# Kernel optimization log

Hardware: AMD Instinct MI355X
Metric: run time of the kernel (lower is better)

The kernel has to match this reference:

```python
import jax, jax.numpy as jnp
import numpy as np

VOCAB = 100000
EMBED = 300
HIDDEN = 300
BATCH = 32768
K_NEG = 10
N_CLASSES = 2
EPS = 1e-5
DENO_W = 1.0
CONO_W = 1.0


def setup_inputs() -> dict:
    key = jax.random.key(0)
    ks = jax.random.split(key, 12)
    init_range = 1.0 / EMBED
    return {
        "center_word_ids": jax.random.randint(ks[0], (BATCH,), 0, VOCAB),
        "context_word_ids": jax.random.randint(ks[1], (BATCH,), 0, VOCAB),
        "neg_context_ids": jax.random.randint(ks[2], (BATCH, K_NEG), 0, VOCAB),
        "party_label": jax.random.randint(ks[3], (BATCH,), 0, N_CLASSES),
        "center_emb": jax.random.uniform(ks[4], (VOCAB, EMBED), jnp.float32, -init_range, init_range),
        "context_emb": jax.random.normal(ks[5], (VOCAB, EMBED), jnp.float32) * 0.02,
        "W_enc": jax.random.normal(ks[6], (HIDDEN, EMBED), jnp.float32) * (1.0 / np.sqrt(EMBED)),
        "b_enc": jnp.zeros((HIDDEN,), jnp.float32),
        "W_dec": jax.random.normal(ks[7], (EMBED, HIDDEN), jnp.float32) * (1.0 / np.sqrt(HIDDEN)),
        "b_dec": jnp.zeros((EMBED,), jnp.float32),
        "W_cls": jax.random.normal(ks[8], (N_CLASSES, HIDDEN), jnp.float32) * (1.0 / np.sqrt(HIDDEN)),
        "b_cls": jnp.zeros((N_CLASSES,), jnp.float32),
    }


def reference(center_word_ids, context_word_ids, neg_context_ids, party_label,
              center_emb, context_emb, W_enc, b_enc, W_dec, b_dec, W_cls, b_cls):
    # encoder_forward (dropout p=0 -> identity)
    emb = center_emb[center_word_ids]                      # [B, E]
    enc = emb @ W_enc.T + b_enc                            # [B, H]
    # deno_forward: skip-gram negative sampling
    center_v = enc @ W_dec.T + b_dec                       # [B, E]
    ctx_v = context_emb[context_word_ids]                  # [B, E]
    pos_score = jnp.clip(jnp.sum(center_v * ctx_v, axis=1), -10.0, 10.0)
    pos = -jax.nn.log_sigmoid(pos_score)                   # [B]
    neg_v = context_emb[neg_context_ids]                   # [B, K, E]
    neg_score = jnp.clip(jnp.einsum('bke,be->bk', neg_v, center_v), -10.0, 10.0)
    neg = -jnp.sum(jax.nn.log_sigmoid(-neg_score), axis=1)  # [B]
    deno_loss = jnp.clip(jnp.mean(pos + neg), EPS, 10.0)
    # cono_forward + cross entropy
    logits = enc @ W_cls.T + b_cls                         # [B, C]
    logp = jax.nn.log_softmax(logits, axis=-1)
    nll = -jnp.take_along_axis(logp, party_label[:, None], axis=1)[:, 0]
    cono_loss = jnp.clip(jnp.mean(nll), EPS, 10.0)
    encoder_loss = jnp.clip(DENO_W * deno_loss + CONO_W * cono_loss, EPS, None)
    return jnp.stack([encoder_loss, deno_loss, cono_loss])
```

## Files before the change

kernel.cpp:

```cpp
#include <hip/hip_runtime.h>
#include <math.h>

#define VOCAB   100000
#define EMBED   300
#define HIDDEN  300
#define BATCH   32768
#define K_NEG   10
#define EPSV    1e-5f

#define KPAD      320
#define NPAD      384
#define CV_STRIDE 304
#define CTX8_STRIDE 304
#define WC2_STRIDE 304
#define FP8_SCALE 64.0f
#define FP8_DESCALE 0.015625f
#define NBUCKET 512

typedef __attribute__((ext_vector_type(8))) short  short8;
typedef __attribute__((ext_vector_type(4))) float  f32x4;
typedef __attribute__((ext_vector_type(2))) float  floatx2;

#if defined(__has_builtin)
#if __has_builtin(__builtin_amdgcn_cvt_pk_f32_fp8) && __has_builtin(__builtin_amdgcn_cvt_pk_fp8_f32)
#define HAVE_CVT_FP8 1
#endif
#endif

__device__ inline float b2f(unsigned short u) {
    union { unsigned int i; float f; } v; v.i = ((unsigned int)u) << 16; return v.f;
}
__device__ inline unsigned short f2b(float f) {
    union { float f; unsigned int i; } v; v.f = f;
    unsigned int r = v.i + 0x7FFFu + ((v.i >> 16) & 1u);
    return (unsigned short)(r >> 16);
}
__device__ inline void up2(unsigned int u, float& lo, float& hi) {
    union { unsigned int i; float f; } a, b;
    a.i = u << 16; b.i = u & 0xFFFF0000u;
    lo = a.f; hi = b.f;
}
__device__ inline float softplus_fast(float x) {
    const float t = __builtin_amdgcn_exp2f(fabsf(x) * -1.44269504f);
    const float l = __builtin_amdgcn_logf(1.f + t) * 0.69314718f;
    return fmaxf(x, 0.f) + l;
}

__device__ inline float fp8_to_f(unsigned int u8) {
    const unsigned s = (u8 >> 7) & 1, e = (u8 >> 3) & 15, m = u8 & 7;
    float v;
    if (e) { union { unsigned i; float f; } b; b.i = ((e + 120u) << 23) | (m << 20); v = b.f; }
    else v = (float)m * 0.001953125f;
    return s ? -v : v;
}
__device__ inline unsigned char f_to_fp8(float x) {
    union { float f; unsigned i; } b; b.f = x;
    const unsigned s = (b.i >> 31) << 7;
    const float a = fabsf(x);
    if (a >= 440.f) return (unsigned char)(s | 0x7E);
    if (a < 0.015625f) {
        int m = (int)rintf(a * 512.f);
        return (unsigned char)(m >= 8 ? (s | 0x08) : (s | (unsigned)m));
    }
    unsigned r = (b.i & 0x7FFFFFFFu) + 0x7FFFFu + ((b.i >> 20) & 1u);
    unsigned e8 = (r >> 23) - 120u;
    unsigned m8 = (r >> 20) & 7u;
    if (e8 > 15u) return (unsigned char)(s | 0x7E);
    return (unsigned char)(s | (e8 << 3) | m8);
}
__device__ inline unsigned enc4fp8(float a, float b, float c, float d) {
#ifdef HAVE_CVT_FP8
    int v = 0;
    v = __builtin_amdgcn_cvt_pk_fp8_f32(a, b, v, false);
    v = __builtin_amdgcn_cvt_pk_fp8_f32(c, d, v, true);
    return (unsigned)v;
#else
    return (unsigned)f_to_fp8(a) | ((unsigned)f_to_fp8(b) << 8) |
           ((unsigned)f_to_fp8(c) << 16) | ((unsigned)f_to_fp8(d) << 24);
#endif
}
__device__ inline void dec4fp8(unsigned u, float* f) {
#ifdef HAVE_CVT_FP8
    floatx2 lo = __builtin_amdgcn_cvt_pk_f32_fp8((int)u, false);
    floatx2 hi = __builtin_amdgcn_cvt_pk_f32_fp8((int)u, true);
    f[0] = lo[0]; f[1] = lo[1]; f[2] = hi[0]; f[3] = hi[1];
#else
    f[0] = fp8_to_f(u); f[1] = fp8_to_f(u >> 8);
    f[2] = fp8_to_f(u >> 16); f[3] = fp8_to_f(u >> 24);
#endif
}

__device__ inline void load_lds16(const void* g, void* l) {
    __builtin_amdgcn_global_load_lds(
        (const __attribute__((address_space(1))) unsigned int*)g,
        (__attribute__((address_space(3))) unsigned int*)l, 16, 0, 0);
}

__device__ inline float red64(float v) {
    #pragma unroll
    for (int m = 32; m; m >>= 1) v += __shfl_xor(v, m);
    return v;
}

__device__ inline unsigned packbf2(float lo, float hi) {
    union { float f; unsigned i; } a, b; a.f = lo; b.f = hi;
    return (b.i & 0xFFFF0000u) | (a.i >> 16);
}

#define NE (BATCH * 40)
#define NC (VOCAB * 19)

__global__ __launch_bounds__(256)
void prep_kernel(const float* __restrict__ cemb, const int* __restrict__ cids,
                 const float* __restrict__ xemb,
                 unsigned short* __restrict__ emb_b, unsigned char* __restrict__ ctx8)
{
    const int gid = blockIdx.x * 256 + threadIdx.x;
    if (gid < NE) {
        const int row = gid / 40;
        const int c8  = (gid - row * 40) * 8;
        const float* src = cemb + (size_t)cids[row] * 300;
        unsigned short t[8];
        if (c8 + 7 < 300) {
            float4 a = *(const float4*)(src + c8);
            float4 b = *(const float4*)(src + c8 + 4);
            t[0]=f2b(a.x); t[1]=f2b(a.y); t[2]=f2b(a.z); t[3]=f2b(a.w);
            t[4]=f2b(b.x); t[5]=f2b(b.y); t[6]=f2b(b.z); t[7]=f2b(b.w);
        } else {
            #pragma unroll
            for (int j = 0; j < 8; ++j) {
                const int c = c8 + j;
                t[j] = (c < 300) ? f2b(src[c]) : (unsigned short)0;
            }
        }
        *(uint4*)(emb_b + (size_t)row * KPAD + c8) = *(const uint4*)t;
    } else if (gid < NE + NC) {
        const int g3  = gid - NE;
        const int row = g3 / 19;
        const int l   = g3 - row * 19;
        const int e0  = l * 16;
        const float* src = xemb + (size_t)row * 300 + e0;
        float v[16];
        #pragma unroll
        for (int q = 0; q < 4; ++q) {
            if (e0 + q * 4 + 3 < 300) {
                float4 a = *(const float4*)(src + q * 4);
                v[q*4+0]=a.x; v[q*4+1]=a.y; v[q*4+2]=a.z; v[q*4+3]=a.w;
            } else {
                #pragma unroll
                for (int j = 0; j < 4; ++j) {
                    const int e = e0 + q * 4 + j;
                    v[q*4+j] = (e < 300) ? src[q*4+j] : 0.f;
                }
            }
        }
        unsigned u[4];
        #pragma unroll
        for (int q = 0; q < 4; ++q)
            u[q] = enc4fp8(v[q*4]*FP8_SCALE, v[q*4+1]*FP8_SCALE,
                           v[q*4+2]*FP8_SCALE, v[q*4+3]*FP8_SCALE);
        *(uint4*)(ctx8 + (size_t)row * CTX8_STRIDE + e0) = make_uint4(u[0],u[1],u[2],u[3]);
    }
}

__global__ __launch_bounds__(256)
void w2_kernel(const float* __restrict__ Wd, const float* __restrict__ We,
               unsigned short* __restrict__ w2p)
{
    __shared__ float ds[16][33];
    __shared__ float es[32][17];
    const int tid = threadIdx.x;
    const int tn = tid >> 4, tk = tid & 15;
    const int n = blockIdx.y * 16 + tn;
    const int k = blockIdx.x * 16 + tk;

    float acc = 0.f;
    for (int h0 = 0; h0 < 300; h0 += 32) {
        {
            const int i = tid * 2;
            const int a = i >> 5, h = i & 31;
            const int rr = blockIdx.y * 16 + a;
            #pragma unroll
            for (int j = 0; j < 2; ++j) {
                const int hh = h + j;
                ds[a][hh] = (rr < 300 && h0 + hh < 300) ? Wd[rr * 300 + h0 + hh] : 0.f;
            }
        }
        {
            const int i = tid * 2;
            const int h = i >> 4, c = i & 15;
            const int cc = blockIdx.x * 16 + c;
            #pragma unroll
            for (int j = 0; j < 2; ++j)
                es[h][c + j] = (h0 + h < 300 && cc + j < 300) ? We[(h0 + h) * 300 + cc + j] : 0.f;
        }
        __syncthreads();
        #pragma unroll
        for (int h = 0; h < 32; ++h)
            acc = fmaf(ds[tn][h], es[h][tk], acc);
        __syncthreads();
    }
    if (n < NPAD && k < KPAD)
        w2p[n * KPAD + k] = (n < 300 && k < 300) ? f2b(acc) : (unsigned short)0;
}

__global__ __launch_bounds__(256)
void wb_kernel(const float* __restrict__ Wd, const float* __restrict__ We,
               const float* __restrict__ Wc, const float* __restrict__ b_enc,
               const float* __restrict__ b_dec, const float* __restrict__ b_cls,
               float* __restrict__ wc2, float* __restrict__ bias2, float* __restrict__ bc2)
{
    const int unit = blockIdx.x * 4 + (threadIdx.x >> 6);
    const int lane = threadIdx.x & 63;
    if (unit >= 914) return;
    float s = 0.f;
    if (unit < 304) {
        const int c = unit;
        if (c < 300)
            for (int k = lane; k < 300; k += 64) s = fmaf(Wd[c * 300 + k], b_enc[k], s);
        s = red64(s);
        if (lane == 0) bias2[c] = (c < 300) ? s + b_dec[c] : 0.f;
    } else if (unit < 912) {
        const int u2 = unit - 304;
        const int j = u2 >= 304 ? 1 : 0;
        const int c = u2 - j * 304;
        if (c < 300)
            for (int h = lane; h < 300; h += 64) s = fmaf(Wc[j * 300 + h], We[h * 300 + c], s);
        s = red64(s);
        if (lane == 0) wc2[j * WC2_STRIDE + c] = s;
    } else {
        const int j = unit - 912;
        for (int h = lane; h < 300; h += 64) s = fmaf(Wc[j * 300 + h], b_enc[h], s);
        s = red64(s);
        if (lane == 0) bc2[j] = s + b_cls[j];
    }
}

__global__ __launch_bounds__(256)
void gemm_cv_kernel(const unsigned short* __restrict__ A,
                    const unsigned short* __restrict__ B,
                    const float* __restrict__ bias,
                    unsigned short* __restrict__ C)
{
    __shared__ unsigned short As[2][128 * 32];
    __shared__ unsigned short Bs[2][128 * 32];

    const int tid  = threadIdx.x;
    const int wave = tid >> 6;
    const int lane = tid & 63;
    const int m0 = blockIdx.y * 128;
    const int n0 = blockIdx.x * 128;

    const int wr = (wave & 1) * 64;
    const int wc = (wave >> 1) * 64;
    const int fr = lane & 15;
    const int fq = lane >> 4;

    const unsigned short* gA[2];
    const unsigned short* gB[2];
    int ldsOff[2];
    #pragma unroll
    for (int inst = 0; inst < 2; ++inst) {
        const int t = wave * 2 + inst;
        const int r = (t << 4) + (lane >> 2);
        const int c = ((lane & 3) - r - (r >> 2)) & 3;
        gA[inst] = A + (size_t)(m0 + r) * KPAD + c * 8;
        gB[inst] = B + (size_t)(n0 + r) * KPAD + c * 8;
        ldsOff[inst] = t << 9;
    }

    int aoff[4], boff[4];
    #pragma unroll
    for (int i = 0; i < 4; ++i) {
        const int ra = wr + i * 16 + fr;
        aoff[i] = (ra << 5) + (((fq + ra + (ra >> 2)) & 3) << 3);
        const int rb = wc + i * 16 + fr;
        boff[i] = (rb << 5) + (((fq + rb + (rb >> 2)) & 3) << 3);
    }

    f32x4 acc[4][4] = {};

    #pragma unroll
    for (int inst = 0; inst < 2; ++inst) {
        load_lds16(gA[inst], &As[0][ldsOff[inst]]);
        load_lds16(gB[inst], &Bs[0][ldsOff[inst]]);
    }

    int cur = 0;
    for (int ki = 0; ki < KPAD / 32; ++ki) {
        __syncthreads();
        if (ki + 1 < KPAD / 32) {
            const int k0 = (ki + 1) * 32;
            #pragma unroll
            for (int inst = 0; inst < 2; ++inst) {
                load_lds16(gA[inst] + k0, &As[cur ^ 1][ldsOff[inst]]);
                load_lds16(gB[inst] + k0, &Bs[cur ^ 1][ldsOff[inst]]);
            }
        }
        short8 af[4], bf[4];
        #pragma unroll
        for (int i = 0; i < 4; ++i) af[i] = *(const short8*)&As[cur][aoff[i]];
        #pragma unroll
        for (int j = 0; j < 4; ++j) bf[j] = *(const short8*)&Bs[cur][boff[j]];
        #pragma unroll
        for (int i = 0; i < 4; ++i)
            #pragma unroll
            for (int j = 0; j < 4; ++j)
                acc[i][j] = __builtin_amdgcn_mfma_f32_16x16x32_bf16(
                    af[i], bf[j], acc[i][j], 0, 0, 0);
        cur ^= 1;
    }

    #pragma unroll
    for (int i = 0; i < 4; ++i) {
        #pragma unroll
        for (int r = 0; r < 4; ++r) {
            const int m = m0 + wr + i * 16 + fq * 4 + r;
            unsigned short* crow = C + (size_t)m * CV_STRIDE;
            #pragma unroll
            for (int j = 0; j < 4; ++j) {
                const int n = n0 + wc + j * 16 + fr;
                if (n < 300) {
                    crow[n] = f2b(acc[i][j][r] + bias[n]);
                } else if (n < CV_STRIDE) {
                    crow[n] = 0;
                }
            }
        }
    }
}

__global__ __launch_bounds__(256)
void score_kernel(const unsigned short* __restrict__ cvb,
                  const unsigned char* __restrict__ ctx8,
                  const int* __restrict__ ctx_ids, const int* __restrict__ neg_ids,
                  float* __restrict__ db)
{
    const int wid  = threadIdx.x >> 6;
    const int lane = threadIdx.x & 63;
    const int fr = lane & 15;
    const int fq = lane >> 4;
    const int r0 = (blockIdx.x * 4 + wid) * 16;
    const int myrow = r0 + fr;

    union { uint4 u; short8 v; } z16; z16.u = make_uint4(0, 0, 0, 0);

    short8 af[10];
    const unsigned short* arow = cvb + (size_t)myrow * CV_STRIDE + fq * 8;
    #pragma unroll
    for (int kk = 0; kk < 10; ++kk) {
        if (kk < 9 || fq < 2) af[kk] = *(const short8*)(arow + kk * 32);
        else af[kk] = z16.v;
    }

    int ids[11];
    ids[0] = ctx_ids[myrow];
    #pragma unroll
    for (int j = 0; j < 10; ++j) ids[j + 1] = neg_ids[myrow * K_NEG + j];

    const bool dlane = (fr >> 2) == fq;
    const int  dreg  = fr & 3;
    float loss = 0.f;

    #pragma unroll
    for (int j = 0; j < 11; ++j) {
        const unsigned char* brow = ctx8 + (size_t)ids[j] * CTX8_STRIDE + fq * 8;
        f32x4 acc = {};
        #pragma unroll
        for (int kk = 0; kk < 10; ++kk) {
            uint2 u;
            if (kk < 9 || fq < 2) u = *(const uint2*)(brow + kk * 32);
            else u = make_uint2(0, 0);
            float f[8];
            dec4fp8(u.x, f); dec4fp8(u.y, f + 4);
            union { unsigned w[4]; short8 v; } bf;
            bf.w[0] = packbf2(f[0], f[1]);
            bf.w[1] = packbf2(f[2], f[3]);
            bf.w[2] = packbf2(f[4], f[5]);
            bf.w[3] = packbf2(f[6], f[7]);
            acc = __builtin_amdgcn_mfma_f32_16x16x32_bf16(af[kk], bf.v, acc, 0, 0, 0);
        }
        if (dlane) {
            float dv = (dreg & 2) ? ((dreg & 1) ? acc[3] : acc[2])
                                  : ((dreg & 1) ? acc[1] : acc[0]);
            float s = dv * FP8_DESCALE;
            s = fminf(10.f, fmaxf(-10.f, s));
            loss += softplus_fast(j == 0 ? -s : s);
        }
    }

    float v = red64(loss);
    if (lane == 0) atomicAdd(&db[blockIdx.x & (NBUCKET - 1)], v);
}

__global__ __launch_bounds__(256)
void ce_kernel(const unsigned short* __restrict__ embb,
               const int* __restrict__ labels,
               const float* __restrict__ wc2, const float* __restrict__ bc2,
               float* __restrict__ cb)
{
    const int wid  = threadIdx.x >> 6;
    const int lane = threadIdx.x & 63;
    const int l5   = lane & 31;
    const int row  = blockIdx.x * 8 + wid * 2 + (lane >> 5);
    const bool act = l5 < 19;

    const uint4 Z4 = make_uint4(0, 0, 0, 0);
    const char* evp = (const char*)(embb + (size_t)row * KPAD);
    uint4 e0 = act ? *(const uint4*)(evp + l5 * 32)      : Z4;
    uint4 e1 = act ? *(const uint4*)(evp + l5 * 32 + 16) : Z4;
    float ev[16];
    up2(e0.x, ev[0], ev[1]);  up2(e0.y, ev[2], ev[3]);
    up2(e0.z, ev[4], ev[5]);  up2(e0.w, ev[6], ev[7]);
    up2(e1.x, ev[8], ev[9]);  up2(e1.y, ev[10], ev[11]);
    up2(e1.z, ev[12], ev[13]);up2(e1.w, ev[14], ev[15]);

    float p0 = 0.f, p1 = 0.f;
    if (act) {
        const float* w0 = wc2 + l5 * 16;
        const float* w1 = wc2 + WC2_STRIDE + l5 * 16;
        #pragma unroll
        for (int q = 0; q < 4; ++q) {
            float4 a = *(const float4*)(w0 + q * 4);
            float4 c = *(const float4*)(w1 + q * 4);
            p0 = fmaf(ev[q*4], a.x, p0); p0 = fmaf(ev[q*4+1], a.y, p0);
            p0 = fmaf(ev[q*4+2], a.z, p0); p0 = fmaf(ev[q*4+3], a.w, p0);
            p1 = fmaf(ev[q*4], c.x, p1); p1 = fmaf(ev[q*4+1], c.y, p1);
            p1 = fmaf(ev[q*4+2], c.z, p1); p1 = fmaf(ev[q*4+3], c.w, p1);
        }
    }
    #pragma unroll
    for (int m = 16; m; m >>= 1) { p0 += __shfl_xor(p0, m); p1 += __shfl_xor(p1, m); }

    if (l5 == 0) {
        const float l0 = p0 + bc2[0];
        const float l1 = p1 + bc2[1];
        const float mx = fmaxf(l0, l1);
        const float lse = mx + logf(expf(l0 - mx) + expf(l1 - mx));
        const float nll = lse - (labels[row] ? l1 : l0);
        atomicAdd(&cb[blockIdx.x & (NBUCKET - 1)], nll);
    }
}

__device__ inline float wave_red64(float v) {
    #pragma unroll
    for (int o = 32; o; o >>= 1) v += __shfl_down(v, o);
    return v;
}
__global__ __launch_bounds__(256)
void finalize_kernel(const float* __restrict__ db, const float* __restrict__ cb,
                     float* __restrict__ out)
{
    const int t = threadIdx.x;
    float d = db[t] + db[t + 256];
    float c = cb[t] + cb[t + 256];
    d = wave_red64(d); c = wave_red64(c);
    __shared__ float sd[4], sc[4];
    if ((t & 63) == 0) { sd[t >> 6] = d; sc[t >> 6] = c; }
    __syncthreads();
    if (t == 0) {
        const float inv = 1.0f / (float)BATCH;
        float deno = (sd[0] + sd[1] + sd[2] + sd[3]) * inv;
        float cono = (sc[0] + sc[1] + sc[2] + sc[3]) * inv;
        deno = fminf(10.f, fmaxf(EPSV, deno));
        cono = fminf(10.f, fmaxf(EPSV, cono));
        out[0] = fmaxf(EPSV, deno + cono);
        out[1] = deno;
        out[2] = cono;
    }
}

extern "C" void kernel_launch(void* const* d_in, const int* in_sizes, int n_in,
                              void* d_out, int out_size, void* d_ws, size_t ws_size,
                              hipStream_t stream)
{
    const int*   cids  = (const int*)d_in[0];
    const int*   ctx   = (const int*)d_in[1];
    const int*   neg   = (const int*)d_in[2];
    const int*   lab   = (const int*)d_in[3];
    const float* cemb  = (const float*)d_in[4];
    const float* xemb  = (const float*)d_in[5];
    const float* W_enc = (const float*)d_in[6];
    const float* b_enc = (const float*)d_in[7];
    const float* W_dec = (const float*)d_in[8];
    const float* b_dec = (const float*)d_in[9];
    const float* W_cls = (const float*)d_in[10];
    const float* b_cls = (const float*)d_in[11];
    float* out = (float*)d_out;

    unsigned short* emb_b = (unsigned short*)d_ws;
    unsigned short* cv_b  = emb_b + (size_t)BATCH * KPAD;
    unsigned char*  ctx8  = (unsigned char*)(cv_b + (size_t)BATCH * CV_STRIDE);
    unsigned short* w2p   = (unsigned short*)(ctx8 + (size_t)VOCAB * CTX8_STRIDE);
    float* wc2   = (float*)(w2p + (size_t)NPAD * KPAD);
    float* bias2 = wc2 + 2 * WC2_STRIDE;
    float* bc2   = bias2 + WC2_STRIDE;
    float* db    = bc2 + 4;
    float* cb    = db + NBUCKET;

    hipMemsetAsync(db, 0, 2 * NBUCKET * sizeof(float), stream);

    prep_kernel<<<(NE + NC + 255) / 256, 256, 0, stream>>>(cemb, cids, xemb, emb_b, ctx8);

    dim3 wgrid(KPAD / 16, NPAD / 16);
    w2_kernel<<<wgrid, 256, 0, stream>>>(W_dec, W_enc, w2p);
    wb_kernel<<<229, 256, 0, stream>>>(W_dec, W_enc, W_cls, b_enc, b_dec, b_cls,
                                       wc2, bias2, bc2);

    dim3 ggrid(3, BATCH / 128);
    gemm_cv_kernel<<<ggrid, 256, 0, stream>>>(emb_b, w2p, bias2, cv_b);

    score_kernel<<<BATCH / 64, 256, 0, stream>>>(cv_b, ctx8, ctx, neg, db);
    ce_kernel<<<BATCH / 8, 256, 0, stream>>>(emb_b, lab, wc2, bc2, cb);

    finalize_kernel<<<1, 256, 0, stream>>>(db, cb, out);
}
```

Baseline: 354.6 us.

## Rewrite prep kernel as grid-stride float4 chunk loop with coalesced loads

The prep kernel now splits both the center-embedding gather and the context-table fp8 conversion into 4-float chunks. A fixed grid of 2048 blocks walks these chunks with a grid-stride loop, issuing four independent loads per thread before converting and storing. Each thread reads one contiguous float4, so a wavefront covers a contiguous span, and more loads are in flight per thread. In exchange, stores become narrower (8-byte or 4-byte), padding is written only by the last chunk of each row, and the index math uses a division by 75. The packbf2 helper in the score kernel is also inlined by hand, which is likely code-neutral.

```diff
diff --git a/kernel.cpp b/kernel.cpp
--- a/kernel.cpp
+++ b/kernel.cpp
@@ -102,64 +102,68 @@
     return v;
 }
 
-__device__ inline unsigned packbf2(float lo, float hi) {
-    union { float f; unsigned i; } a, b; a.f = lo; b.f = hi;
-    return (b.i & 0xFFFF0000u) | (a.i >> 16);
-}
-
-#define NE (BATCH * 40)
-#define NC (VOCAB * 19)
+#define CH1 (BATCH * 75)
+#define CH2 (VOCAB * 75)
+#define CHTOT (CH1 + CH2)
+#define PREP_BLOCKS 2048
 
 __global__ __launch_bounds__(256)
 void prep_kernel(const float* __restrict__ cemb, const int* __restrict__ cids,
                  const float* __restrict__ xemb,
                  unsigned short* __restrict__ emb_b, unsigned char* __restrict__ ctx8)
 {
-    const int gid = blockIdx.x * 256 + threadIdx.x;
-    if (gid < NE) {
-        const int row = gid / 40;
-        const int c8  = (gid - row * 40) * 8;
-        const float* src = cemb + (size_t)cids[row] * 300;
-        unsigned short t[8];
-        if (c8 + 7 < 300) {
-            float4 a = *(const float4*)(src + c8);
-            float4 b = *(const float4*)(src + c8 + 4);
-            t[0]=f2b(a.x); t[1]=f2b(a.y); t[2]=f2b(a.z); t[3]=f2b(a.w);
-            t[4]=f2b(b.x); t[5]=f2b(b.y); t[6]=f2b(b.z); t[7]=f2b(b.w);
-        } else {
-            #pragma unroll
-            for (int j = 0; j < 8; ++j) {
-                const int c = c8 + j;
-                t[j] = (c < 300) ? f2b(src[c]) : (unsigned short)0;
-            }
-        }
-        *(uint4*)(emb_b + (size_t)row * KPAD + c8) = *(const uint4*)t;
-    } else if (gid < NE + NC) {
-        const int g3  = gid - NE;
-        const int row = g3 / 19;
-        const int l   = g3 - row * 19;
-        const int e0  = l * 16;
-        const float* src = xemb + (size_t)row * 300 + e0;
-        float v[16];
-        #pragma unroll
-        for (int q = 0; q < 4; ++q) {
-            if (e0 + q * 4 + 3 < 300) {
-                float4 a = *(const float4*)(src + q * 4);
-                v[q*4+0]=a.x; v[q*4+1]=a.y; v[q*4+2]=a.z; v[q*4+3]=a.w;
-            } else {
-                #pragma unroll
-                for (int j = 0; j < 4; ++j) {
-                    const int e = e0 + q * 4 + j;
-                    v[q*4+j] = (e < 300) ? src[q*4+j] : 0.f;
+    const unsigned GT = PREP_BLOCKS * 256;
+    for (unsigned base = blockIdx.x * 256 + threadIdx.x; base < CHTOT; base += GT * 4) {
+        float4 v[4];
+        unsigned c[4];
+        bool ok[4];
+        #pragma unroll
+        for (int u = 0; u < 4; ++u) {
+            c[u] = base + u * GT;
+            ok[u] = (c[u] < CHTOT);
+            if (ok[u]) {
+                unsigned cc = c[u];
+                if (cc < CH1) {
+                    const unsigned row = cc / 75, e = cc - row * 75;
+                    v[u] = *(const float4*)(cemb + (size_t)cids[row] * 300 + e * 4);
+                } else {
+                    cc -= CH1;
+                    const unsigned row = cc / 75, e = cc - row * 75;
+                    v[u] = *(const float4*)(xemb + (size_t)row * 300 + e * 4);
                 }
             }
         }
-        unsigned u[4];
-        #pragma unroll
-        for (int q = 0; q < 4; ++q)
-            u[q] = enc4fp8(v[q*4]*FP8_SCALE, v[q*4+1]*FP8_SCALE,
-                           v[q*4+2]*FP8_SCALE, v[q*4+3]*FP8_SCALE);
-        *(uint4*)(ctx8 + (size_t)row * CTX8_STRIDE + e0) = make_uint4(u[0],u[1],u[2],u[3]);
+        #pragma unroll
+        for (int u = 0; u < 4; ++u) {
+            if (!ok[u]) continue;
+            unsigned cc = c[u];
+            if (cc < CH1) {
+                const unsigned row = cc / 75, e = cc - row * 75;
+                uint2 d;
+                d.x = (unsigned)f2b(v[u].x) | ((unsigned)f2b(v[u].y) << 16);
+                d.y = (unsigned)f2b(v[u].z) | ((unsigned)f2b(v[u].w) << 16);
+                char* dst = (char*)emb_b + (size_t)row * (KPAD * 2) + e * 8;
+                if (e < 74) {
+                    *(uint2*)dst = d;
+                } else {
+                    *(uint4*)dst = make_uint4(d.x, d.y, 0u, 0u);
+                    char* rb = (char*)emb_b + (size_t)row * (KPAD * 2);
+                    *(uint4*)(rb + 608) = make_uint4(0u, 0u, 0u, 0u);
+                    *(uint4*)(rb + 624) = make_uint4(0u, 0u, 0u, 0u);
+                }
+            } else {
+                cc -= CH1;
+                const unsigned row = cc / 75, e = cc - row * 75;
+                const unsigned enc = enc4fp8(v[u].x * FP8_SCALE, v[u].y * FP8_SCALE,
+                                             v[u].z * FP8_SCALE, v[u].w * FP8_SCALE);
+                char* dst = (char*)ctx8 + (size_t)row * CTX8_STRIDE + e * 4;
+                if (e < 74) {
+                    *(unsigned*)dst = enc;
+                } else {
+                    *(uint2*)dst = make_uint2(enc, 0u);
+                }
+            }
+        }
     }
 }
 
@@ -374,10 +378,13 @@
             float f[8];
             dec4fp8(u.x, f); dec4fp8(u.y, f + 4);
             union { unsigned w[4]; short8 v; } bf;
-            bf.w[0] = packbf2(f[0], f[1]);
-            bf.w[1] = packbf2(f[2], f[3]);
-            bf.w[2] = packbf2(f[4], f[5]);
-            bf.w[3] = packbf2(f[6], f[7]);
+            union { float ff; unsigned ii; } p0, p1, p2, p3, p4, p5, p6, p7;
+            p0.ff = f[0]; p1.ff = f[1]; p2.ff = f[2]; p3.ff = f[3];
+            p4.ff = f[4]; p5.ff = f[5]; p6.ff = f[6]; p7.ff = f[7];
+            bf.w[0] = (p1.ii & 0xFFFF0000u) | (p0.ii >> 16);
+            bf.w[1] = (p3.ii & 0xFFFF0000u) | (p2.ii >> 16);
+            bf.w[2] = (p5.ii & 0xFFFF0000u) | (p4.ii >> 16);
+            bf.w[3] = (p7.ii & 0xFFFF0000u) | (p6.ii >> 16);
             acc = __builtin_amdgcn_mfma_f32_16x16x32_bf16(af[kk], bf.v, acc, 0, 0, 0);
         }
         if (dlane) {
@@ -500,7 +507,7 @@
 
     hipMemsetAsync(db, 0, 2 * NBUCKET * sizeof(float), stream);
 
-    prep_kernel<<<(NE + NC + 255) / 256, 256, 0, stream>>>(cemb, cids, xemb, emb_b, ctx8);
+    prep_kernel<<<PREP_BLOCKS, 256, 0, stream>>>(cemb, cids, xemb, emb_b, ctx8);
 
     dim3 wgrid(KPAD / 16, NPAD / 16);
     w2_kernel<<<wgrid, 256, 0, stream>>>(W_dec, W_enc, w2p);
```

Result: no change. 360.9 us (+1.8%).
